# Performance work log

Measured on AMD Instinct MI355X. Metric: run time of the kernel, lower is better.

## Reference

```python
import jax, jax.numpy as jnp
import numpy as np

B, L, D, H, HID = 2048, 512, 17, 8, 256  # batch, max entities, feat dim, heads, mlp hidden
SPECIAL, OUT = 9, 23  # special vector dims, policy logits (7+16)


def _lin(k, out_d, in_d, scale):
    kw, kb = jax.random.split(k)
    W = jax.random.normal(kw, (out_d, in_d), jnp.float32) * scale
    b = jax.random.normal(kb, (out_d,), jnp.float32) * 0.01
    return W, b


def setup_inputs() -> dict:
    key = jax.random.key(0)
    ks = jax.random.split(key, 16)
    # observations: row 0 holds the 9-dim special vector, rows 1..L are ragged entities
    x = jax.random.normal(ks[0], (B, L + 1, D), jnp.float32)
    lengths = jax.random.randint(ks[1], (B,), 1, L + 1)
    mask = (jnp.arange(L)[None, :] < lengths[:, None]).astype(jnp.float32)
    x = x.at[:, 1:, :].multiply(mask[:, :, None])  # zero rows mark padding
    s = 1.0 / np.sqrt(D)
    # per-head K/V projections (num_heads separate tiny Linears)
    Wk = jax.random.normal(ks[2], (H, D, D), jnp.float32) * s
    bk = jax.random.normal(ks[3], (H, D), jnp.float32) * 0.01
    Wv = jax.random.normal(ks[4], (H, D, D), jnp.float32) * s
    bv = jax.random.normal(ks[5], (H, D), jnp.float32) * 0.01
    q = jax.random.normal(ks[6], (H, D), jnp.float32)  # learned per-head queries
    Wo, bo = _lin(ks[7], D, H * D, 1.0 / np.sqrt(H * D))
    sc = 1.0 / np.sqrt(D + SPECIAL)
    pW1, pb1 = _lin(ks[8], HID, D + SPECIAL, sc)
    pW2, pb2 = _lin(ks[9], HID, HID, 1.0 / np.sqrt(HID))
    pW3, pb3 = _lin(ks[10], OUT, HID, 1.0 / np.sqrt(HID))
    vW1, vb1 = _lin(ks[11], HID, D + SPECIAL, sc)
    vW2, vb2 = _lin(ks[12], HID, HID, 1.0 / np.sqrt(HID))
    vW3, vb3 = _lin(ks[13], 1, HID, 1.0 / np.sqrt(HID))
    return dict(x=x, Wk=Wk, bk=bk, Wv=Wv, bv=bv, q=q, Wo=Wo, bo=bo,
                pW1=pW1, pb1=pb1, pW2=pW2, pb2=pb2, pW3=pW3, pb3=pb3,
                vW1=vW1, vb1=vb1, vW2=vW2, vb2=vb2, vW3=vW3, vb3=vb3)


def _mlp(h, W1, b1, W2, b2, W3, b3):
    h = jax.nn.relu(h @ W1.T + b1)
    h = jax.nn.relu(h @ W2.T + b2)
    return h @ W3.T + b3


def reference(x, Wk, bk, Wv, bv, q, Wo, bo,
              pW1, pb1, pW2, pb2, pW3, pb3,
              vW1, vb1, vW2, vb2, vW3, vb3):
    special = x[:, 0, :SPECIAL]            # [B, 9]
    seq = x[:, 1:, :]                      # [B, L, D]
    mask = jnp.sum(jnp.abs(seq), axis=-1) != 0  # [B, L] non-padded rows
    # per-head keys/values for all samples at once (batched over the head loop)
    keys = jnp.einsum('bld,hed->bhle', seq, Wk) + bk[None, :, None, :]   # [B,H,L,D]
    vals = jnp.einsum('bld,hed->bhle', seq, Wv) + bv[None, :, None, :]   # [B,H,L,D]
    scores = jnp.einsum('bhle,he->bhl', keys, q)                          # [B,H,L]
    scores = jnp.where(mask[:, None, :], scores, -1e9)
    w = jax.nn.softmax(scores, axis=-1)                                   # [B,H,L]
    agg = jnp.einsum('bhl,bhle->bhe', w, vals).reshape(x.shape[0], H * D)  # concat heads
    attn = agg @ Wo.T + bo                                                # [B, D]
    comb = jnp.concatenate([attn, special], axis=-1)                      # [B, D+9]
    logits = _mlp(comb, pW1, pb1, pW2, pb2, pW3, pb3)                     # [B, 23]
    value = _mlp(comb, vW1, vb1, vW2, vb2, vW3, vb3)                      # [B, 1]
    return logits, value
```

## Files before the change

### kernel.cpp

```cpp
#include <hip/hip_runtime.h>
#include <hip/hip_bf16.h>

#define B_ 2048
#define D_ 17
#define H_ 8
#define HID_ 256
#define OUT_ 23
#define XROW 8721
#define SEQN 8704
#define LAST4 4465151

typedef unsigned int u32;
typedef const __attribute__((address_space(1))) u32* gp1_t;
typedef __attribute__((address_space(3))) u32* lp3_t;

__device__ __forceinline__ float bclane(float v, int l) {
  return __uint_as_float(__builtin_amdgcn_readlane(__float_as_uint(v), l));
}

__device__ __forceinline__ void gload_lds16(const float4* gsrc_lane, float* lds_wave_base) {
  __builtin_amdgcn_global_load_lds((gp1_t)(const void*)gsrc_lane,
                                   (lp3_t)(void*)lds_wave_base, 16, 0, 0);
}

__global__ __launch_bounds__(256) void prep_kernel(
    const float* __restrict__ pW2, const float* __restrict__ vW2,
    const float* __restrict__ Wk, const float* __restrict__ bk,
    const float* __restrict__ q,
    float* __restrict__ pW2t, float* __restrict__ vW2t, float* __restrict__ qkc)
{
  const int bid = blockIdx.x;
  const int t = threadIdx.x;
  if (bid == 128) {
    if (t < H_ * D_) {
      const int h = t / D_, dd = t - h * D_;
      float s = 0.f;
      #pragma unroll
      for (int e = 0; e < D_; ++e) s = fmaf(Wk[h*289 + e*D_ + dd], q[h*D_ + e], s);
      qkc[h*18 + dd] = s;
    } else if (t < H_ * D_ + H_) {
      const int h = t - H_ * D_;
      float s = 0.f;
      #pragma unroll
      for (int e = 0; e < D_; ++e) s = fmaf(bk[h*D_ + e], q[h*D_ + e], s);
      qkc[h*18 + 17] = s;
    }
    return;
  }
  __shared__ float tile[32][33];
  const int m = bid >> 6, tid = bid & 63;
  const int ti = (tid >> 3) * 32, tk = (tid & 7) * 32;
  const float* src = m ? vW2 : pW2;
  float* dst = m ? vW2t : pW2t;
  const int tx = t & 31, ty = t >> 5;
  #pragma unroll
  for (int r = 0; r < 4; ++r) tile[ty + 8*r][tx] = src[(ti + ty + 8*r)*HID_ + tk + tx];
  __syncthreads();
  #pragma unroll
  for (int r = 0; r < 4; ++r) dst[(tk + ty + 8*r)*HID_ + ti + tx] = tile[tx][ty + 8*r];
}

__global__ __launch_bounds__(256, 4) void attn_comb_kernel(
    const float* __restrict__ x, const float* __restrict__ qkc,
    const float* __restrict__ Wv, const float* __restrict__ bv,
    const float* __restrict__ Wo, const float* __restrict__ bo,
    float* __restrict__ comb)
{
  __shared__ __align__(16) float s_seq[9216];
  __shared__ float s_part[4][H_][18];
  __shared__ float s_swn[136];
  __shared__ float s_agg[136];
  __shared__ float s_wp[136];

  const int t = threadIdx.x;
  const int b = blockIdx.x;
  const int w = t >> 6, lane = t & 63;
  const int hp = lane >> 4;
  const int rg = lane & 15;
  const int seq0 = b * XROW + D_;
  const int s4 = seq0 >> 2;
  const int phase = seq0 & 3;
  const float4* __restrict__ x4 = (const float4*)x;

  const float pv = x[seq0 + lane * 136];

  {
    float* dstb = s_seq + ((t & ~63) << 2);
    const int g0 = s4 + t;
    gload_lds16(x4 + g0,          dstb);
    gload_lds16(x4 + g0 + 256,    dstb + 1024);
    gload_lds16(x4 + g0 + 512,    dstb + 2048);
    gload_lds16(x4 + g0 + 768,    dstb + 3072);
    gload_lds16(x4 + g0 + 1024,   dstb + 4096);

    const unsigned long long live = __ballot(pv != 0.f) | 1ull;
    const int nr = 8 * (64 - __builtin_clzll(live));
    const int rounds = min(9, (nr * D_ + phase + 1023) >> 10);

    if (rounds > 5) gload_lds16(x4 + g0 + 1280, dstb + 5120);
    if (rounds > 6) gload_lds16(x4 + g0 + 1536, dstb + 6144);
    if (rounds > 7) gload_lds16(x4 + g0 + 1792, dstb + 7168);
    if (rounds > 8) gload_lds16(x4 + min(g0 + 2048, LAST4), dstb + 8192);
  }
  const unsigned long long live2 = __ballot(pv != 0.f) | 1ull;
  const int nrows = 8 * (64 - __builtin_clzll(live2));

  const float* q0 = qkc + (2*hp) * 18;
  float qk0[D_], qk1[D_];
  #pragma unroll
  for (int d = 0; d < D_; ++d) { qk0[d] = q0[d]; qk1[d] = q0[18 + d]; }
  const float ch0 = q0[17], ch1 = q0[35];

  __syncthreads();

  float den0 = 0.f, den1 = 0.f;
  float acc0[D_], acc1[D_];
  #pragma unroll
  for (int d = 0; d < D_; ++d) { acc0[d] = 0.f; acc1[d] = 0.f; }

  auto dorow = [&](int row) {
    const float* rp = &s_seq[phase + row * D_];
    const float f0 = rp[0],  f1 = rp[1],  f2 = rp[2],  f3 = rp[3];
    const float f4 = rp[4],  f5 = rp[5],  f6 = rp[6],  f7 = rp[7];
    const float f8 = rp[8],  f9 = rp[9],  f10 = rp[10], f11 = rp[11];
    const float f12 = rp[12], f13 = rp[13], f14 = rp[14], f15 = rp[15];
    const float f16 = rp[16];
    float sA = ch0, sB = ch1;
    sA = fmaf(qk0[0],  f0,  sA); sB = fmaf(qk1[0],  f0,  sB);
    sA = fmaf(qk0[1],  f1,  sA); sB = fmaf(qk1[1],  f1,  sB);
    sA = fmaf(qk0[2],  f2,  sA); sB = fmaf(qk1[2],  f2,  sB);
    sA = fmaf(qk0[3],  f3,  sA); sB = fmaf(qk1[3],  f3,  sB);
    sA = fmaf(qk0[4],  f4,  sA); sB = fmaf(qk1[4],  f4,  sB);
    sA = fmaf(qk0[5],  f5,  sA); sB = fmaf(qk1[5],  f5,  sB);
    sA = fmaf(qk0[6],  f6,  sA); sB = fmaf(qk1[6],  f6,  sB);
    sA = fmaf(qk0[7],  f7,  sA); sB = fmaf(qk1[7],  f7,  sB);
    sA = fmaf(qk0[8],  f8,  sA); sB = fmaf(qk1[8],  f8,  sB);
    sA = fmaf(qk0[9],  f9,  sA); sB = fmaf(qk1[9],  f9,  sB);
    sA = fmaf(qk0[10], f10, sA); sB = fmaf(qk1[10], f10, sB);
    sA = fmaf(qk0[11], f11, sA); sB = fmaf(qk1[11], f11, sB);
    sA = fmaf(qk0[12], f12, sA); sB = fmaf(qk1[12], f12, sB);
    sA = fmaf(qk0[13], f13, sA); sB = fmaf(qk1[13], f13, sB);
    sA = fmaf(qk0[14], f14, sA); sB = fmaf(qk1[14], f14, sB);
    sA = fmaf(qk0[15], f15, sA); sB = fmaf(qk1[15], f15, sB);
    sA = fmaf(qk0[16], f16, sA); sB = fmaf(qk1[16], f16, sB);
    const bool lv = (row < nrows) && (f0 != 0.f);
    const float p0 = lv ? __expf(sA) : 0.f;
    const float p1 = lv ? __expf(sB) : 0.f;
    den0 += p0; den1 += p1;
    acc0[0]  = fmaf(p0, f0,  acc0[0]);  acc1[0]  = fmaf(p1, f0,  acc1[0]);
    acc0[1]  = fmaf(p0, f1,  acc0[1]);  acc1[1]  = fmaf(p1, f1,  acc1[1]);
    acc0[2]  = fmaf(p0, f2,  acc0[2]);  acc1[2]  = fmaf(p1, f2,  acc1[2]);
    acc0[3]  = fmaf(p0, f3,  acc0[3]);  acc1[3]  = fmaf(p1, f3,  acc1[3]);
    acc0[4]  = fmaf(p0, f4,  acc0[4]);  acc1[4]  = fmaf(p1, f4,  acc1[4]);
    acc0[5]  = fmaf(p0, f5,  acc0[5]);  acc1[5]  = fmaf(p1, f5,  acc1[5]);
    acc0[6]  = fmaf(p0, f6,  acc0[6]);  acc1[6]  = fmaf(p1, f6,  acc1[6]);
    acc0[7]  = fmaf(p0, f7,  acc0[7]);  acc1[7]  = fmaf(p1, f7,  acc1[7]);
    acc0[8]  = fmaf(p0, f8,  acc0[8]);  acc1[8]  = fmaf(p1, f8,  acc1[8]);
    acc0[9]  = fmaf(p0, f9,  acc0[9]);  acc1[9]  = fmaf(p1, f9,  acc1[9]);
    acc0[10] = fmaf(p0, f10, acc0[10]); acc1[10] = fmaf(p1, f10, acc1[10]);
    acc0[11] = fmaf(p0, f11, acc0[11]); acc1[11] = fmaf(p1, f11, acc1[11]);
    acc0[12] = fmaf(p0, f12, acc0[12]); acc1[12] = fmaf(p1, f12, acc1[12]);
    acc0[13] = fmaf(p0, f13, acc0[13]); acc1[13] = fmaf(p1, f13, acc1[13]);
    acc0[14] = fmaf(p0, f14, acc0[14]); acc1[14] = fmaf(p1, f14, acc1[14]);
    acc0[15] = fmaf(p0, f15, acc0[15]); acc1[15] = fmaf(p1, f15, acc1[15]);
    acc0[16] = fmaf(p0, f16, acc0[16]); acc1[16] = fmaf(p1, f16, acc1[16]);
  };

  {
    const int s0r = w * 64;
    if (s0r < nrows) {
      dorow(s0r + rg);
      dorow(s0r + rg + 16);
      dorow(s0r + rg + 32);
      dorow(s0r + rg + 48);
    }
    const int s1r = 256 + w * 64;
    if (s1r < nrows) {
      dorow(s1r + rg);
      dorow(s1r + rg + 16);
      dorow(s1r + rg + 32);
      dorow(s1r + rg + 48);
    }
  }

  #pragma unroll
  for (int m = 1; m <= 8; m <<= 1) {
    den0 += __shfl_xor(den0, m, 64);
    den1 += __shfl_xor(den1, m, 64);
    #pragma unroll
    for (int d = 0; d < D_; ++d) {
      acc0[d] += __shfl_xor(acc0[d], m, 64);
      acc1[d] += __shfl_xor(acc1[d], m, 64);
    }
  }
  if (rg == 0) {
    float* p0p = &s_part[w][2*hp][0];
    float* p1p = &s_part[w][2*hp + 1][0];
    p0p[0] = den0; p1p[0] = den1;
    #pragma unroll
    for (int d = 0; d < D_; ++d) { p0p[1 + d] = acc0[d]; p1p[1 + d] = acc1[d]; }
  }
  __syncthreads();

  if (t < 136) {
    const int hh = t / D_, d = t - hh * D_;
    float dn = 0.f, ac = 0.f;
    #pragma unroll
    for (int ww = 0; ww < 4; ++ww) { dn += s_part[ww][hh][0]; ac += s_part[ww][hh][1 + d]; }
    s_swn[t] = ac / dn;
  }
  __syncthreads();
  if (t < 136) {
    const int hh = t / D_, e = t - hh * D_;
    float s = bv[t];
    #pragma unroll
    for (int d = 0; d < D_; ++d) s = fmaf(Wv[hh*289 + e*D_ + d], s_swn[hh*D_ + d], s);
    s_agg[t] = s;
  }
  __syncthreads();
  if (t < 136) {
    const int o = t >> 3, pt = t & 7;
    float s = 0.f;
    #pragma unroll
    for (int j = 0; j < D_; ++j) s = fmaf(Wo[o*136 + pt*D_ + j], s_agg[pt*D_ + j], s);
    s_wp[t] = s;
  }
  __syncthreads();
  if (t < D_) {
    float s = bo[t];
    #pragma unroll
    for (int pt = 0; pt < 8; ++pt) s += s_wp[t*8 + pt];
    comb[b*26 + t] = s;
  } else if (t < 26) {
    comb[b*26 + t] = x[b * XROW + (t - D_)];
  }
}

__global__ __launch_bounds__(512) void mlp_kernel(
    const float* __restrict__ comb,
    const float* __restrict__ pW1, const float* __restrict__ pb1,
    const float* __restrict__ pW2t, const float* __restrict__ pb2,
    const float* __restrict__ pW3, const float* __restrict__ pb3,
    const float* __restrict__ vW1, const float* __restrict__ vb1,
    const float* __restrict__ vW2t, const float* __restrict__ vb2,
    const float* __restrict__ vW3, const float* __restrict__ vb3,
    float* __restrict__ out)
{
  __shared__ float s_comb[8][26];
  __shared__ __align__(16) float s_red[2][3][8][HID_];
  __shared__ __align__(16) float s_h2[2][8][HID_];

  const int t = threadIdx.x;
  const int b0 = blockIdx.x * 8;
  const int p = t >> 8;
  const int kq = (t >> 6) & 3;
  const int ln = t & 63;

  if (t < 208) { const int bb = t / 26, k = t - bb*26; s_comb[bb][k] = comb[(size_t)(b0 + bb)*26 + k]; }
  __syncthreads();

  const float* W1  = p ? vW1  : pW1;   const float* B1 = p ? vb1 : pb1;
  const float* W2t = p ? vW2t : pW2t;  const float* B2 = p ? vb2 : pb2;

  float h[8];
  {
    const int i = kq * 64 + ln;
    float a[8];
    #pragma unroll
    for (int bb = 0; bb < 8; ++bb) a[bb] = 0.f;
    const float* wr = W1 + i * 26;
    for (int k = 0; k < 26; ++k) {
      const float wk = wr[k];
      #pragma unroll
      for (int bb = 0; bb < 8; ++bb) a[bb] = fmaf(wk, s_comb[bb][k], a[bb]);
    }
    const float bias = B1[i];
    #pragma unroll
    for (int bb = 0; bb < 8; ++bb) h[bb] = fmaxf(a[bb] + bias, 0.f);
  }

  float4 acc[8];
  #pragma unroll
  for (int bb = 0; bb < 8; ++bb) acc[bb] = make_float4(0.f, 0.f, 0.f, 0.f);
  {
    const float* wbase = W2t + (size_t)(kq * 64) * HID_ + 4 * ln;
    #pragma unroll 8
    for (int jj = 0; jj < 64; ++jj) {
      const float4 wv = *(const float4*)(wbase + (size_t)jj * HID_);
      #pragma unroll
      for (int bb = 0; bb < 8; ++bb) {
        const float hv = bclane(h[bb], jj);
        acc[bb].x = fmaf(wv.x, hv, acc[bb].x);
        acc[bb].y = fmaf(wv.y, hv, acc[bb].y);
        acc[bb].z = fmaf(wv.z, hv, acc[bb].z);
        acc[bb].w = fmaf(wv.w, hv, acc[bb].w);
      }
    }
  }
  if (kq > 0) {
    #pragma unroll
    for (int bb = 0; bb < 8; ++bb) *(float4*)&s_red[p][kq - 1][bb][4 * ln] = acc[bb];
  }
  __syncthreads();
  if (kq == 0) {
    const float4 bias = *(const float4*)&B2[4 * ln];
    #pragma unroll
    for (int bb = 0; bb < 8; ++bb) {
      const float4 r0 = *(const float4*)&s_red[p][0][bb][4 * ln];
      const float4 r1 = *(const float4*)&s_red[p][1][bb][4 * ln];
      const float4 r2 = *(const float4*)&s_red[p][2][bb][4 * ln];
      float4 rr;
      rr.x = fmaxf(acc[bb].x + r0.x + r1.x + r2.x + bias.x, 0.f);
      rr.y = fmaxf(acc[bb].y + r0.y + r1.y + r2.y + bias.y, 0.f);
      rr.z = fmaxf(acc[bb].z + r0.z + r1.z + r2.z + bias.z, 0.f);
      rr.w = fmaxf(acc[bb].w + r0.w + r1.w + r2.w + bias.w, 0.f);
      *(float4*)&s_h2[p][bb][4 * ln] = rr;
    }
  }
  __syncthreads();

  if (t < 184) {
    const int bb = t / OUT_, o = t - bb * OUT_;
    const float4* w4 = (const float4*)(pW3 + o * HID_);
    const float4* h4 = (const float4*)&s_h2[0][bb][0];
    float s = pb3[o];
    for (int k = 0; k < 64; ++k) {
      const float4 wv = w4[k], hv = h4[k];
      s = fmaf(wv.x, hv.x, fmaf(wv.y, hv.y, fmaf(wv.z, hv.z, fmaf(wv.w, hv.w, s))));
    }
    out[(size_t)(b0 + bb) * OUT_ + o] = s;
  } else if (t >= 256 && t < 264) {
    const int bb = t - 256;
    const float4* w4 = (const float4*)vW3;
    const float4* h4 = (const float4*)&s_h2[1][bb][0];
    float s = vb3[0];
    for (int k = 0; k < 64; ++k) {
      const float4 wv = w4[k], hv = h4[k];
      s = fmaf(wv.x, hv.x, fmaf(wv.y, hv.y, fmaf(wv.z, hv.z, fmaf(wv.w, hv.w, s))));
    }
    out[(size_t)B_ * OUT_ + b0 + bb] = s;
  }
}

extern "C" void kernel_launch(void* const* d_in, const int* in_sizes, int n_in,
                              void* d_out, int out_size, void* d_ws, size_t ws_size,
                              hipStream_t stream) {
  (void)in_sizes; (void)n_in; (void)out_size; (void)ws_size;
  const float* x   = (const float*)d_in[0];
  const float* Wk  = (const float*)d_in[1];
  const float* bk  = (const float*)d_in[2];
  const float* Wv  = (const float*)d_in[3];
  const float* bv  = (const float*)d_in[4];
  const float* q   = (const float*)d_in[5];
  const float* Wo  = (const float*)d_in[6];
  const float* bo  = (const float*)d_in[7];
  const float* pW1 = (const float*)d_in[8];
  const float* pb1 = (const float*)d_in[9];
  const float* pW2 = (const float*)d_in[10];
  const float* pb2 = (const float*)d_in[11];
  const float* pW3 = (const float*)d_in[12];
  const float* pb3 = (const float*)d_in[13];
  const float* vW1 = (const float*)d_in[14];
  const float* vb1 = (const float*)d_in[15];
  const float* vW2 = (const float*)d_in[16];
  const float* vb2 = (const float*)d_in[17];
  const float* vW3 = (const float*)d_in[18];
  const float* vb3 = (const float*)d_in[19];
  float* out = (float*)d_out;

  float* pW2t = (float*)d_ws;
  float* vW2t = pW2t + (size_t)HID_ * HID_;
  float* qkc  = vW2t + (size_t)HID_ * HID_;
  float* comb = qkc + 160;

  prep_kernel<<<129, 256, 0, stream>>>(pW2, vW2, Wk, bk, q, pW2t, vW2t, qkc);
  attn_comb_kernel<<<B_, 256, 0, stream>>>(x, qkc, Wv, bv, Wo, bo, comb);
  mlp_kernel<<<B_ / 8, 512, 0, stream>>>(comb, pW1, pb1, pW2t, pb2, pW3, pb3,
                                         vW1, vb1, vW2t, vb2, vW3, vb3, out);
}
```

Measured before the change: 52.72 us.

## Persistent attention blocks with double-buffered LDS prefetch of next sample

The attention kernel now launches 512 blocks, each handling 4 samples in a loop. It double-buffers the LDS sequence tile so the async global-to-LDS loads for the next sample are issued while the current one is computed. All four samples' live-row counts are found up front, so every load round, including the first five, is skipped when unneeded. This hides load latency within a block, but the LDS footprint doubles, the launch bound drops to 2 blocks per CU and there are fewer blocks overall, so occupancy-based latency hiding goes down.

After: 57.60 us. 9.2% more time.

```diff
diff --git a/kernel.cpp b/kernel.cpp
--- a/kernel.cpp
+++ b/kernel.cpp
@@ -60,50 +60,32 @@
   for (int r = 0; r < 4; ++r) dst[(tk + ty + 8*r)*HID_ + ti + tx] = tile[tx][ty + 8*r];
 }
 
-__global__ __launch_bounds__(256, 4) void attn_comb_kernel(
+__global__ __launch_bounds__(256, 2) void attn_comb_kernel(
     const float* __restrict__ x, const float* __restrict__ qkc,
     const float* __restrict__ Wv, const float* __restrict__ bv,
     const float* __restrict__ Wo, const float* __restrict__ bo,
     float* __restrict__ comb)
 {
-  __shared__ __align__(16) float s_seq[9216];
+  __shared__ __align__(16) float s_buf[2][9216];
   __shared__ float s_part[4][H_][18];
   __shared__ float s_swn[136];
   __shared__ float s_agg[136];
   __shared__ float s_wp[136];
+  __shared__ int s_nr[4];
 
   const int t = threadIdx.x;
-  const int b = blockIdx.x;
+  const int bid = blockIdx.x;
   const int w = t >> 6, lane = t & 63;
   const int hp = lane >> 4;
   const int rg = lane & 15;
-  const int seq0 = b * XROW + D_;
-  const int s4 = seq0 >> 2;
-  const int phase = seq0 & 3;
   const float4* __restrict__ x4 = (const float4*)x;
 
-  const float pv = x[seq0 + lane * 136];
-
   {
-    float* dstb = s_seq + ((t & ~63) << 2);
-    const int g0 = s4 + t;
-    gload_lds16(x4 + g0,          dstb);
-    gload_lds16(x4 + g0 + 256,    dstb + 1024);
-    gload_lds16(x4 + g0 + 512,    dstb + 2048);
-    gload_lds16(x4 + g0 + 768,    dstb + 3072);
-    gload_lds16(x4 + g0 + 1024,   dstb + 4096);
-
+    const int bw = bid + (w << 9);
+    const float pv = x[bw * XROW + D_ + lane * 136];
     const unsigned long long live = __ballot(pv != 0.f) | 1ull;
-    const int nr = 8 * (64 - __builtin_clzll(live));
-    const int rounds = min(9, (nr * D_ + phase + 1023) >> 10);
-
-    if (rounds > 5) gload_lds16(x4 + g0 + 1280, dstb + 5120);
-    if (rounds > 6) gload_lds16(x4 + g0 + 1536, dstb + 6144);
-    if (rounds > 7) gload_lds16(x4 + g0 + 1792, dstb + 7168);
-    if (rounds > 8) gload_lds16(x4 + min(g0 + 2048, LAST4), dstb + 8192);
-  }
-  const unsigned long long live2 = __ballot(pv != 0.f) | 1ull;
-  const int nrows = 8 * (64 - __builtin_clzll(live2));
+    if (lane == 0) s_nr[w] = 8 * (64 - __builtin_clzll(live));
+  }
 
   const float* q0 = qkc + (2*hp) * 18;
   float qk0[D_], qk1[D_];
@@ -113,126 +95,160 @@
 
   __syncthreads();
 
-  float den0 = 0.f, den1 = 0.f;
-  float acc0[D_], acc1[D_];
-  #pragma unroll
-  for (int d = 0; d < D_; ++d) { acc0[d] = 0.f; acc1[d] = 0.f; }
-
-  auto dorow = [&](int row) {
-    const float* rp = &s_seq[phase + row * D_];
-    const float f0 = rp[0],  f1 = rp[1],  f2 = rp[2],  f3 = rp[3];
-    const float f4 = rp[4],  f5 = rp[5],  f6 = rp[6],  f7 = rp[7];
-    const float f8 = rp[8],  f9 = rp[9],  f10 = rp[10], f11 = rp[11];
-    const float f12 = rp[12], f13 = rp[13], f14 = rp[14], f15 = rp[15];
-    const float f16 = rp[16];
-    float sA = ch0, sB = ch1;
-    sA = fmaf(qk0[0],  f0,  sA); sB = fmaf(qk1[0],  f0,  sB);
-    sA = fmaf(qk0[1],  f1,  sA); sB = fmaf(qk1[1],  f1,  sB);
-    sA = fmaf(qk0[2],  f2,  sA); sB = fmaf(qk1[2],  f2,  sB);
-    sA = fmaf(qk0[3],  f3,  sA); sB = fmaf(qk1[3],  f3,  sB);
-    sA = fmaf(qk0[4],  f4,  sA); sB = fmaf(qk1[4],  f4,  sB);
-    sA = fmaf(qk0[5],  f5,  sA); sB = fmaf(qk1[5],  f5,  sB);
-    sA = fmaf(qk0[6],  f6,  sA); sB = fmaf(qk1[6],  f6,  sB);
-    sA = fmaf(qk0[7],  f7,  sA); sB = fmaf(qk1[7],  f7,  sB);
-    sA = fmaf(qk0[8],  f8,  sA); sB = fmaf(qk1[8],  f8,  sB);
-    sA = fmaf(qk0[9],  f9,  sA); sB = fmaf(qk1[9],  f9,  sB);
-    sA = fmaf(qk0[10], f10, sA); sB = fmaf(qk1[10], f10, sB);
-    sA = fmaf(qk0[11], f11, sA); sB = fmaf(qk1[11], f11, sB);
-    sA = fmaf(qk0[12], f12, sA); sB = fmaf(qk1[12], f12, sB);
-    sA = fmaf(qk0[13], f13, sA); sB = fmaf(qk1[13], f13, sB);
-    sA = fmaf(qk0[14], f14, sA); sB = fmaf(qk1[14], f14, sB);
-    sA = fmaf(qk0[15], f15, sA); sB = fmaf(qk1[15], f15, sB);
-    sA = fmaf(qk0[16], f16, sA); sB = fmaf(qk1[16], f16, sB);
-    const bool lv = (row < nrows) && (f0 != 0.f);
-    const float p0 = lv ? __expf(sA) : 0.f;
-    const float p1 = lv ? __expf(sB) : 0.f;
-    den0 += p0; den1 += p1;
-    acc0[0]  = fmaf(p0, f0,  acc0[0]);  acc1[0]  = fmaf(p1, f0,  acc1[0]);
-    acc0[1]  = fmaf(p0, f1,  acc0[1]);  acc1[1]  = fmaf(p1, f1,  acc1[1]);
-    acc0[2]  = fmaf(p0, f2,  acc0[2]);  acc1[2]  = fmaf(p1, f2,  acc1[2]);
-    acc0[3]  = fmaf(p0, f3,  acc0[3]);  acc1[3]  = fmaf(p1, f3,  acc1[3]);
-    acc0[4]  = fmaf(p0, f4,  acc0[4]);  acc1[4]  = fmaf(p1, f4,  acc1[4]);
-    acc0[5]  = fmaf(p0, f5,  acc0[5]);  acc1[5]  = fmaf(p1, f5,  acc1[5]);
-    acc0[6]  = fmaf(p0, f6,  acc0[6]);  acc1[6]  = fmaf(p1, f6,  acc1[6]);
-    acc0[7]  = fmaf(p0, f7,  acc0[7]);  acc1[7]  = fmaf(p1, f7,  acc1[7]);
-    acc0[8]  = fmaf(p0, f8,  acc0[8]);  acc1[8]  = fmaf(p1, f8,  acc1[8]);
-    acc0[9]  = fmaf(p0, f9,  acc0[9]);  acc1[9]  = fmaf(p1, f9,  acc1[9]);
-    acc0[10] = fmaf(p0, f10, acc0[10]); acc1[10] = fmaf(p1, f10, acc1[10]);
-    acc0[11] = fmaf(p0, f11, acc0[11]); acc1[11] = fmaf(p1, f11, acc1[11]);
-    acc0[12] = fmaf(p0, f12, acc0[12]); acc1[12] = fmaf(p1, f12, acc1[12]);
-    acc0[13] = fmaf(p0, f13, acc0[13]); acc1[13] = fmaf(p1, f13, acc1[13]);
-    acc0[14] = fmaf(p0, f14, acc0[14]); acc1[14] = fmaf(p1, f14, acc1[14]);
-    acc0[15] = fmaf(p0, f15, acc0[15]); acc1[15] = fmaf(p1, f15, acc1[15]);
-    acc0[16] = fmaf(p0, f16, acc0[16]); acc1[16] = fmaf(p1, f16, acc1[16]);
+  auto stage_issue = [&](int j) {
+    const int bj = bid + (j << 9);
+    const int seq0 = bj * XROW + D_;
+    const int s4 = seq0 >> 2;
+    const int phase = seq0 & 3;
+    const int rounds = min(9, (s_nr[j] * D_ + phase + 1023) >> 10);
+    float* dstb = s_buf[j & 1] + ((t & ~63) << 2);
+    const int g0 = s4 + t;
+    gload_lds16(x4 + g0, dstb);
+    if (rounds > 1) gload_lds16(x4 + g0 +  256, dstb + 1024);
+    if (rounds > 2) gload_lds16(x4 + g0 +  512, dstb + 2048);
+    if (rounds > 3) gload_lds16(x4 + g0 +  768, dstb + 3072);
+    if (rounds > 4) gload_lds16(x4 + g0 + 1024, dstb + 4096);
+    if (rounds > 5) gload_lds16(x4 + g0 + 1280, dstb + 5120);
+    if (rounds > 6) gload_lds16(x4 + g0 + 1536, dstb + 6144);
+    if (rounds > 7) gload_lds16(x4 + g0 + 1792, dstb + 7168);
+    if (rounds > 8) gload_lds16(x4 + min(g0 + 2048, LAST4), dstb + 8192);
   };
 
-  {
-    const int s0r = w * 64;
-    if (s0r < nrows) {
-      dorow(s0r + rg);
-      dorow(s0r + rg + 16);
-      dorow(s0r + rg + 32);
-      dorow(s0r + rg + 48);
-    }
-    const int s1r = 256 + w * 64;
-    if (s1r < nrows) {
-      dorow(s1r + rg);
-      dorow(s1r + rg + 16);
-      dorow(s1r + rg + 32);
-      dorow(s1r + rg + 48);
-    }
-  }
-
-  #pragma unroll
-  for (int m = 1; m <= 8; m <<= 1) {
-    den0 += __shfl_xor(den0, m, 64);
-    den1 += __shfl_xor(den1, m, 64);
-    #pragma unroll
-    for (int d = 0; d < D_; ++d) {
-      acc0[d] += __shfl_xor(acc0[d], m, 64);
-      acc1[d] += __shfl_xor(acc1[d], m, 64);
-    }
-  }
-  if (rg == 0) {
-    float* p0p = &s_part[w][2*hp][0];
-    float* p1p = &s_part[w][2*hp + 1][0];
-    p0p[0] = den0; p1p[0] = den1;
-    #pragma unroll
-    for (int d = 0; d < D_; ++d) { p0p[1 + d] = acc0[d]; p1p[1 + d] = acc1[d]; }
-  }
-  __syncthreads();
-
-  if (t < 136) {
-    const int hh = t / D_, d = t - hh * D_;
-    float dn = 0.f, ac = 0.f;
-    #pragma unroll
-    for (int ww = 0; ww < 4; ++ww) { dn += s_part[ww][hh][0]; ac += s_part[ww][hh][1 + d]; }
-    s_swn[t] = ac / dn;
-  }
-  __syncthreads();
-  if (t < 136) {
-    const int hh = t / D_, e = t - hh * D_;
-    float s = bv[t];
-    #pragma unroll
-    for (int d = 0; d < D_; ++d) s = fmaf(Wv[hh*289 + e*D_ + d], s_swn[hh*D_ + d], s);
-    s_agg[t] = s;
-  }
-  __syncthreads();
-  if (t < 136) {
-    const int o = t >> 3, pt = t & 7;
-    float s = 0.f;
-    #pragma unroll
-    for (int j = 0; j < D_; ++j) s = fmaf(Wo[o*136 + pt*D_ + j], s_agg[pt*D_ + j], s);
-    s_wp[t] = s;
-  }
-  __syncthreads();
-  if (t < D_) {
-    float s = bo[t];
-    #pragma unroll
-    for (int pt = 0; pt < 8; ++pt) s += s_wp[t*8 + pt];
-    comb[b*26 + t] = s;
-  } else if (t < 26) {
-    comb[b*26 + t] = x[b * XROW + (t - D_)];
+  stage_issue(0);
+  __syncthreads();
+
+  #pragma unroll 1
+  for (int j = 0; j < 4; ++j) {
+    if (j + 1 < 4) stage_issue(j + 1);
+
+    const int bj = bid + (j << 9);
+    const int nrows = s_nr[j];
+    const int phase = (bj * XROW + D_) & 3;
+    const float* sb = s_buf[j & 1];
+
+    float den0 = 0.f, den1 = 0.f;
+    float acc0[D_], acc1[D_];
+    #pragma unroll
+    for (int d = 0; d < D_; ++d) { acc0[d] = 0.f; acc1[d] = 0.f; }
+
+    auto dorow = [&](int row) {
+      const int rr = (row < nrows) ? row : 0;
+      const float* rp = &sb[phase + rr * D_];
+      const float f0 = rp[0],  f1 = rp[1],  f2 = rp[2],  f3 = rp[3];
+      const float f4 = rp[4],  f5 = rp[5],  f6 = rp[6],  f7 = rp[7];
+      const float f8 = rp[8],  f9 = rp[9],  f10 = rp[10], f11 = rp[11];
+      const float f12 = rp[12], f13 = rp[13], f14 = rp[14], f15 = rp[15];
+      const float f16 = rp[16];
+      float sA = ch0, sB = ch1;
+      sA = fmaf(qk0[0],  f0,  sA); sB = fmaf(qk1[0],  f0,  sB);
+      sA = fmaf(qk0[1],  f1,  sA); sB = fmaf(qk1[1],  f1,  sB);
+      sA = fmaf(qk0[2],  f2,  sA); sB = fmaf(qk1[2],  f2,  sB);
+      sA = fmaf(qk0[3],  f3,  sA); sB = fmaf(qk1[3],  f3,  sB);
+      sA = fmaf(qk0[4],  f4,  sA); sB = fmaf(qk1[4],  f4,  sB);
+      sA = fmaf(qk0[5],  f5,  sA); sB = fmaf(qk1[5],  f5,  sB);
+      sA = fmaf(qk0[6],  f6,  sA); sB = fmaf(qk1[6],  f6,  sB);
+      sA = fmaf(qk0[7],  f7,  sA); sB = fmaf(qk1[7],  f7,  sB);
+      sA = fmaf(qk0[8],  f8,  sA); sB = fmaf(qk1[8],  f8,  sB);
+      sA = fmaf(qk0[9],  f9,  sA); sB = fmaf(qk1[9],  f9,  sB);
+      sA = fmaf(qk0[10], f10, sA); sB = fmaf(qk1[10], f10, sB);
+      sA = fmaf(qk0[11], f11, sA); sB = fmaf(qk1[11], f11, sB);
+      sA = fmaf(qk0[12], f12, sA); sB = fmaf(qk1[12], f12, sB);
+      sA = fmaf(qk0[13], f13, sA); sB = fmaf(qk1[13], f13, sB);
+      sA = fmaf(qk0[14], f14, sA); sB = fmaf(qk1[14], f14, sB);
+      sA = fmaf(qk0[15], f15, sA); sB = fmaf(qk1[15], f15, sB);
+      sA = fmaf(qk0[16], f16, sA); sB = fmaf(qk1[16], f16, sB);
+      const bool lv = (row < nrows) && (f0 != 0.f);
+      const float p0 = lv ? __expf(sA) : 0.f;
+      const float p1 = lv ? __expf(sB) : 0.f;
+      den0 += p0; den1 += p1;
+      acc0[0]  = fmaf(p0, f0,  acc0[0]);  acc1[0]  = fmaf(p1, f0,  acc1[0]);
+      acc0[1]  = fmaf(p0, f1,  acc0[1]);  acc1[1]  = fmaf(p1, f1,  acc1[1]);
+      acc0[2]  = fmaf(p0, f2,  acc0[2]);  acc1[2]  = fmaf(p1, f2,  acc1[2]);
+      acc0[3]  = fmaf(p0, f3,  acc0[3]);  acc1[3]  = fmaf(p1, f3,  acc1[3]);
+      acc0[4]  = fmaf(p0, f4,  acc0[4]);  acc1[4]  = fmaf(p1, f4,  acc1[4]);
+      acc0[5]  = fmaf(p0, f5,  acc0[5]);  acc1[5]  = fmaf(p1, f5,  acc1[5]);
+      acc0[6]  = fmaf(p0, f6,  acc0[6]);  acc1[6]  = fmaf(p1, f6,  acc1[6]);
+      acc0[7]  = fmaf(p0, f7,  acc0[7]);  acc1[7]  = fmaf(p1, f7,  acc1[7]);
+      acc0[8]  = fmaf(p0, f8,  acc0[8]);  acc1[8]  = fmaf(p1, f8,  acc1[8]);
+      acc0[9]  = fmaf(p0, f9,  acc0[9]);  acc1[9]  = fmaf(p1, f9,  acc1[9]);
+      acc0[10] = fmaf(p0, f10, acc0[10]); acc1[10] = fmaf(p1, f10, acc1[10]);
+      acc0[11] = fmaf(p0, f11, acc0[11]); acc1[11] = fmaf(p1, f11, acc1[11]);
+      acc0[12] = fmaf(p0, f12, acc0[12]); acc1[12] = fmaf(p1, f12, acc1[12]);
+      acc0[13] = fmaf(p0, f13, acc0[13]); acc1[13] = fmaf(p1, f13, acc1[13]);
+      acc0[14] = fmaf(p0, f14, acc0[14]); acc1[14] = fmaf(p1, f14, acc1[14]);
+      acc0[15] = fmaf(p0, f15, acc0[15]); acc1[15] = fmaf(p1, f15, acc1[15]);
+      acc0[16] = fmaf(p0, f16, acc0[16]); acc1[16] = fmaf(p1, f16, acc1[16]);
+    };
+
+    {
+      const int s0r = w * 64;
+      if (s0r < nrows) {
+        dorow(s0r + rg);
+        dorow(s0r + rg + 16);
+        dorow(s0r + rg + 32);
+        dorow(s0r + rg + 48);
+      }
+      const int s1r = 256 + w * 64;
+      if (s1r < nrows) {
+        dorow(s1r + rg);
+        dorow(s1r + rg + 16);
+        dorow(s1r + rg + 32);
+        dorow(s1r + rg + 48);
+      }
+    }
+
+    #pragma unroll
+    for (int m = 1; m <= 8; m <<= 1) {
+      den0 += __shfl_xor(den0, m, 64);
+      den1 += __shfl_xor(den1, m, 64);
+      #pragma unroll
+      for (int d = 0; d < D_; ++d) {
+        acc0[d] += __shfl_xor(acc0[d], m, 64);
+        acc1[d] += __shfl_xor(acc1[d], m, 64);
+      }
+    }
+    if (rg == 0) {
+      float* p0p = &s_part[w][2*hp][0];
+      float* p1p = &s_part[w][2*hp + 1][0];
+      p0p[0] = den0; p1p[0] = den1;
+      #pragma unroll
+      for (int d = 0; d < D_; ++d) { p0p[1 + d] = acc0[d]; p1p[1 + d] = acc1[d]; }
+    }
+    __syncthreads();
+
+    if (t < 136) {
+      const int hh = t / D_, d = t - hh * D_;
+      float dn = 0.f, ac = 0.f;
+      #pragma unroll
+      for (int ww = 0; ww < 4; ++ww) { dn += s_part[ww][hh][0]; ac += s_part[ww][hh][1 + d]; }
+      s_swn[t] = ac / dn;
+    }
+    __syncthreads();
+    if (t < 136) {
+      const int hh = t / D_, e = t - hh * D_;
+      float s = bv[t];
+      #pragma unroll
+      for (int d = 0; d < D_; ++d) s = fmaf(Wv[hh*289 + e*D_ + d], s_swn[hh*D_ + d], s);
+      s_agg[t] = s;
+    }
+    __syncthreads();
+    if (t < 136) {
+      const int o = t >> 3, pt = t & 7;
+      float s = 0.f;
+      #pragma unroll
+      for (int jj = 0; jj < D_; ++jj) s = fmaf(Wo[o*136 + pt*D_ + jj], s_agg[pt*D_ + jj], s);
+      s_wp[t] = s;
+    }
+    __syncthreads();
+    if (t < D_) {
+      float s = bo[t];
+      #pragma unroll
+      for (int pt = 0; pt < 8; ++pt) s += s_wp[t*8 + pt];
+      comb[bj*26 + t] = s;
+    } else if (t < 26) {
+      comb[bj*26 + t] = x[bj * XROW + (t - D_)];
+    }
+    __syncthreads();
   }
 }
 
@@ -374,7 +390,7 @@
   float* comb = qkc + 160;
 
   prep_kernel<<<129, 256, 0, stream>>>(pW2, vW2, Wk, bk, q, pW2t, vW2t, qkc);
-  attn_comb_kernel<<<B_, 256, 0, stream>>>(x, qkc, Wv, bv, Wo, bo, comb);
+  attn_comb_kernel<<<512, 256, 0, stream>>>(x, qkc, Wv, bv, Wo, bo, comb);
   mlp_kernel<<<B_ / 8, 512, 0, stream>>>(comb, pW1, pb1, pW2t, pb2, pW3, pb3,
                                          vW1, vb1, vW2t, vb2, vW3, vb3, out);
 }
```
